# Performance work log

Measured on AMD Instinct MI355X. Metric: run time of the kernel, lower is better.

The kernel has to match this reference:

```python
import jax, jax.numpy as jnp
import numpy as np

X_DIM, H_DIM, Z_DIM = 4096, 4096, 512
EMB_DIM, NUM_EMB = 512, 8192
BATCH = 8192
COMMIT = 0.25


def setup_inputs() -> dict:
    key = jax.random.key(0)
    ks = jax.random.split(key, 12)
    s = 0.02
    return {
        "x": jax.random.normal(ks[0], (BATCH, X_DIM), dtype=jnp.float32),
        "enc_w1": jax.random.normal(ks[1], (X_DIM, H_DIM), dtype=jnp.float32) * s,
        "enc_b1": jnp.zeros((H_DIM,), dtype=jnp.float32),
        "enc_w2": jax.random.normal(ks[2], (H_DIM, Z_DIM), dtype=jnp.float32) * s,
        "enc_b2": jnp.zeros((Z_DIM,), dtype=jnp.float32),
        "pre_w": jax.random.normal(ks[3], (Z_DIM, EMB_DIM), dtype=jnp.float32) * s,
        "pre_b": jnp.zeros((EMB_DIM,), dtype=jnp.float32),
        "codebook": jax.random.normal(ks[4], (NUM_EMB, EMB_DIM), dtype=jnp.float32) * s,
        "dec_w1": jax.random.normal(ks[5], (EMB_DIM, H_DIM), dtype=jnp.float32) * s,
        "dec_b1": jnp.zeros((H_DIM,), dtype=jnp.float32),
        "dec_w2": jax.random.normal(ks[6], (H_DIM, X_DIM), dtype=jnp.float32) * s,
        "dec_b2": jnp.zeros((X_DIM,), dtype=jnp.float32),
    }


def reference(x, enc_w1, enc_b1, enc_w2, enc_b2, pre_w, pre_b, codebook,
              dec_w1, dec_b1, dec_w2, dec_b2):
    # Encoder MLP: Linear -> ReLU -> Linear
    h = jax.nn.relu(x @ enc_w1 + enc_b1)              # [B, H]
    z = h @ enc_w2 + enc_b2                           # [B, Z]
    z_e = z @ pre_w + pre_b                           # [B, E]

    # Vector quantization: nearest codebook entry by L2 distance
    # ||z||^2 - 2 z E^T + ||E||^2 over K codes
    d = (jnp.sum(z_e * z_e, axis=1, keepdims=True)
         - 2.0 * (z_e @ codebook.T)
         + jnp.sum(codebook * codebook, axis=1))      # [B, K]
    idx = jnp.argmin(d, axis=1)                       # [B]
    z_q = codebook[idx]                               # [B, E] gather

    # VQ losses
    e_latent = jnp.mean((jax.lax.stop_gradient(z_q) - z_e) ** 2)
    q_latent = jnp.mean((z_q - jax.lax.stop_gradient(z_e)) ** 2)
    vq_loss = q_latent + COMMIT * e_latent

    # Perplexity of code usage
    counts = jnp.zeros((NUM_EMB,), dtype=jnp.float32).at[idx].add(1.0)
    avg_probs = counts / z_e.shape[0]
    perplexity = jnp.exp(-jnp.sum(avg_probs * jnp.log(avg_probs + 1e-10)))

    # Straight-through estimator
    z_st = z_e + jax.lax.stop_gradient(z_q - z_e)

    # Decoder MLP
    hd = jax.nn.relu(z_st @ dec_w1 + dec_b1)
    x_recon = hd @ dec_w2 + dec_b2                    # [B, X]
    return (x_recon, vq_loss, perplexity)
```

## Files before the change

### kernel.cpp

```cpp
#include <hip/hip_runtime.h>
#include <cstdint>
#include <cstddef>


#define BM 128
#define BN 128
#define BKT 16
#define LDA 132
#define LDB 132

typedef _Float16 half_t;
typedef __attribute__((ext_vector_type(8))) _Float16 f16x8;
typedef __attribute__((ext_vector_type(4))) _Float16 f16x4;
typedef __attribute__((ext_vector_type(4))) float floatx4;
typedef __attribute__((ext_vector_type(8))) short bf16x8;

#define LO_SCALE 4096.f
#define LO_INV   2.44140625e-4f

__device__ __forceinline__ short f2bf(float v) {
    union { float f; unsigned u; } x; x.f = v;
    unsigned r = x.u + 0x7fff + ((x.u >> 16) & 1);
    return (short)(r >> 16);
}

__device__ __forceinline__ void gload16(const void* g, void* l) {
    __builtin_amdgcn_global_load_lds(
        (const __attribute__((address_space(1))) void*)(uintptr_t)g,
        (__attribute__((address_space(3))) void*)(uintptr_t)l,
        16, 0, 0);
}

__device__ __forceinline__ void fsplit(float v, half_t& hi, half_t& lo) {
    hi = (half_t)v;
    lo = (half_t)((v - (float)hi) * LO_SCALE);
}

__global__ __launch_bounds__(256, 2)
void gemm_bias_act(const float* __restrict__ A, const float* __restrict__ B,
                   const float* __restrict__ bias, float* __restrict__ C,
                   int M, int N, int K, int relu)
{
    __shared__ float as[BKT][LDA];
    __shared__ float bs[BKT][LDB];
    const int tid = threadIdx.x;
    const int tx = tid & 15;
    const int ty = tid >> 4;
    const int row0 = blockIdx.y * BM;
    const int col0 = blockIdx.x * BN;

    const int ar = tid >> 2;
    const int ac = (tid & 3) << 2;
    const int br = tid >> 5;
    const int bc = (tid & 31) << 2;

    const float* Ap0 = A + (size_t)(row0 + ar) * K + ac;
    const float* Ap1 = A + (size_t)(row0 + ar + 64) * K + ac;
    const float* Bp0 = B + (size_t)br * N + col0 + bc;
    const float* Bp1 = B + (size_t)(br + 8) * N + col0 + bc;

    float acc[8][8];
#pragma unroll
    for (int i = 0; i < 8; ++i)
#pragma unroll
        for (int j = 0; j < 8; ++j) acc[i][j] = 0.f;

    for (int k0 = 0; k0 < K; k0 += BKT) {
        float4 a0 = *(const float4*)(Ap0 + k0);
        float4 a1 = *(const float4*)(Ap1 + k0);
        float4 b0 = *(const float4*)(Bp0 + (size_t)k0 * N);
        float4 b1 = *(const float4*)(Bp1 + (size_t)k0 * N);
        __syncthreads();
        as[ac + 0][ar] = a0.x; as[ac + 1][ar] = a0.y;
        as[ac + 2][ar] = a0.z; as[ac + 3][ar] = a0.w;
        as[ac + 0][ar + 64] = a1.x; as[ac + 1][ar + 64] = a1.y;
        as[ac + 2][ar + 64] = a1.z; as[ac + 3][ar + 64] = a1.w;
        *(float4*)&bs[br][bc] = b0;
        *(float4*)&bs[br + 8][bc] = b1;
        __syncthreads();
#pragma unroll
        for (int k = 0; k < BKT; ++k) {
            float af[8], bf0[4], bf1[4];
            *(float4*)&af[0] = *(const float4*)&as[k][ty * 8];
            *(float4*)&af[4] = *(const float4*)&as[k][ty * 8 + 4];
            *(float4*)&bf0[0] = *(const float4*)&bs[k][tx * 4];
            *(float4*)&bf1[0] = *(const float4*)&bs[k][64 + tx * 4];
#pragma unroll
            for (int i = 0; i < 8; ++i) {
#pragma unroll
                for (int j = 0; j < 4; ++j) {
                    acc[i][j]     = fmaf(af[i], bf0[j], acc[i][j]);
                    acc[i][j + 4] = fmaf(af[i], bf1[j], acc[i][j + 4]);
                }
            }
        }
    }

    float bv0[4], bv1[4];
#pragma unroll
    for (int j = 0; j < 4; ++j) {
        bv0[j] = bias[col0 + tx * 4 + j];
        bv1[j] = bias[col0 + 64 + tx * 4 + j];
    }
#pragma unroll
    for (int i = 0; i < 8; ++i) {
        const int row = row0 + ty * 8 + i;
        float4 o0, o1;
        o0.x = acc[i][0] + bv0[0]; o0.y = acc[i][1] + bv0[1];
        o0.z = acc[i][2] + bv0[2]; o0.w = acc[i][3] + bv0[3];
        o1.x = acc[i][4] + bv1[0]; o1.y = acc[i][5] + bv1[1];
        o1.z = acc[i][6] + bv1[2]; o1.w = acc[i][7] + bv1[3];
        if (relu) {
            o0.x = fmaxf(o0.x, 0.f); o0.y = fmaxf(o0.y, 0.f);
            o0.z = fmaxf(o0.z, 0.f); o0.w = fmaxf(o0.w, 0.f);
            o1.x = fmaxf(o1.x, 0.f); o1.y = fmaxf(o1.y, 0.f);
            o1.z = fmaxf(o1.z, 0.f); o1.w = fmaxf(o1.w, 0.f);
        }
        *(float4*)(C + (size_t)row * N + col0 + tx * 4) = o0;
        *(float4*)(C + (size_t)row * N + col0 + 64 + tx * 4) = o1;
    }
}

__global__ void cnorm_kernel(const float* __restrict__ CB, float* __restrict__ cnorm, int E)
{
    const int j = blockIdx.x;
    const float* c = CB + (size_t)j * E;
    float s = 0.f;
    for (int e = threadIdx.x; e < E; e += 64) { float v = c[e]; s += v * v; }
#pragma unroll
    for (int off = 32; off; off >>= 1) s += __shfl_down(s, off);
    if (threadIdx.x == 0) cnorm[j] = s;
}

__global__ void argmin_reduce(const float* __restrict__ partv, const int* __restrict__ parti,
                              int* __restrict__ idx, int M, int P)
{
    const int m = blockIdx.x * blockDim.x + threadIdx.x;
    if (m >= M) return;
    const float* pv = partv + (size_t)m * P;
    const int* pi = parti + (size_t)m * P;
    float best = pv[0]; int bi = pi[0];
    for (int t = 1; t < P; ++t) {
        float v = pv[t]; int ii = pi[t];
        if (v < best || (v == best && ii < bi)) { best = v; bi = ii; }
    }
    idx[m] = bi;
}

__global__ __launch_bounds__(256)
void vq_stats(const float* __restrict__ ZE, const float* __restrict__ CB,
              const int* __restrict__ idx, int* __restrict__ counts,
              float* __restrict__ vqaccum, int E)
{
    const int i = blockIdx.x;
    const int id = idx[i];
    const float* c = CB + (size_t)id * E;
    const float* z = ZE + (size_t)i * E;
    float s = 0.f;
    for (int e = threadIdx.x; e < E; e += 256) { float d = c[e] - z[e]; s += d * d; }
#pragma unroll
    for (int off = 32; off; off >>= 1) s += __shfl_down(s, off);
    __shared__ float red[4];
    const int lane = threadIdx.x & 63, w = threadIdx.x >> 6;
    if (lane == 0) red[w] = s;
    __syncthreads();
    if (threadIdx.x == 0) {
        atomicAdd(vqaccum, red[0] + red[1] + red[2] + red[3]);
        atomicAdd(counts + id, 1);
    }
}

__global__ void zero_kernel(int* __restrict__ p, int n)
{
    const int i = blockIdx.x * 256 + threadIdx.x;
    if (i < n) p[i] = 0;
}

__global__ __launch_bounds__(256)
void finalize(const int* __restrict__ counts, const float* __restrict__ vqaccum,
              float* __restrict__ tail, int NCODE, float invB, float scale)
{
    float s = 0.f;
    for (int j = threadIdx.x; j < NCODE; j += 256) {
        float p = (float)counts[j] * invB;
        s += p * logf(p + 1e-10f);
    }
#pragma unroll
    for (int off = 32; off; off >>= 1) s += __shfl_down(s, off);
    __shared__ float red[4];
    const int lane = threadIdx.x & 63, w = threadIdx.x >> 6;
    if (lane == 0) red[w] = s;
    __syncthreads();
    if (threadIdx.x == 0) {
        tail[0] = vqaccum[0] * scale;
        tail[1] = expf(-(red[0] + red[1] + red[2] + red[3]));
    }
}

__global__ __launch_bounds__(256)
void transpose_bf16(const float* __restrict__ src, short* __restrict__ dst,
                    int Kd, int Nd)
{
    __shared__ float tile[32][33];
    const int bx = blockIdx.x * 32;
    const int by = blockIdx.y * 32;
    const int tx = threadIdx.x & 31, ty = threadIdx.x >> 5;
#pragma unroll
    for (int i = ty; i < 32; i += 8)
        tile[i][tx] = src[(size_t)(by + i) * Nd + bx + tx];
    __syncthreads();
#pragma unroll
    for (int i = ty; i < 32; i += 8)
        dst[(size_t)(bx + i) * Kd + by + tx] = f2bf(tile[tx][i]);
}

__global__ __launch_bounds__(256)
void transpose_split2(const float* __restrict__ src, half_t* __restrict__ dh,
                      half_t* __restrict__ dl, int Kd, int Nd)
{
    __shared__ float tile[32][33];
    const int bx = blockIdx.x * 32;
    const int by = blockIdx.y * 32;
    const int tx = threadIdx.x & 31, ty = threadIdx.x >> 5;
#pragma unroll
    for (int i = ty; i < 32; i += 8)
        tile[i][tx] = src[(size_t)(by + i) * Nd + bx + tx];
    __syncthreads();
#pragma unroll
    for (int i = ty; i < 32; i += 8) {
        float v = tile[tx][i];
        half_t h, l; fsplit(v, h, l);
        dh[(size_t)(bx + i) * Kd + by + tx] = h;
        dl[(size_t)(bx + i) * Kd + by + tx] = l;
    }
}

__global__ void convert_bf16_vec(const float* __restrict__ src, short* __restrict__ dst, int n4)
{
    const int i = blockIdx.x * 256 + threadIdx.x;
    if (i >= n4) return;
    float4 v = ((const float4*)src)[i];
    short4 o;
    o.x = f2bf(v.x); o.y = f2bf(v.y); o.z = f2bf(v.z); o.w = f2bf(v.w);
    ((short4*)dst)[i] = o;
}

__global__ void split2_vec(const float* __restrict__ src, half_t* __restrict__ hi,
                           half_t* __restrict__ lo, int n4)
{
    const int i = blockIdx.x * 256 + threadIdx.x;
    if (i >= n4) return;
    float4 v = ((const float4*)src)[i];
    f16x4 h, l;
    h[0] = (half_t)v.x; l[0] = (half_t)((v.x - (float)h[0]) * LO_SCALE);
    h[1] = (half_t)v.y; l[1] = (half_t)((v.y - (float)h[1]) * LO_SCALE);
    h[2] = (half_t)v.z; l[2] = (half_t)((v.z - (float)h[2]) * LO_SCALE);
    h[3] = (half_t)v.w; l[3] = (half_t)((v.w - (float)h[3]) * LO_SCALE);
    ((f16x4*)hi)[i] = h;
    ((f16x4*)lo)[i] = l;
}

template<int MODE>
__global__ __launch_bounds__(256, 2)
void gemm_f16x2(const half_t* __restrict__ Ah, const half_t* __restrict__ Al,
                const half_t* __restrict__ Bh, const half_t* __restrict__ Bl,
                const float* __restrict__ bias, float* __restrict__ Cf,
                half_t* __restrict__ Ch, half_t* __restrict__ Cl,
                int N, int K)
{
    __shared__ half_t sAh[128 * 32], sAl[128 * 32], sBh[128 * 32], sBl[128 * 32];
    const int t = threadIdx.x;
    const int lane = t & 63, wave = t >> 6;
    const int rh = (wave >> 1) * 64, ch = (wave & 1) * 64;
    const int ml = lane & 15, quad = lane >> 4;
    const int row0 = blockIdx.y * 128, col0 = blockIdx.x * 128;

    const int r = t >> 2, c = t & 3;
    const half_t* pA0h = Ah + (size_t)(row0 + r) * K + c * 8;
    const half_t* pA1h = Ah + (size_t)(row0 + r + 64) * K + c * 8;
    const half_t* pA0l = Al + (size_t)(row0 + r) * K + c * 8;
    const half_t* pA1l = Al + (size_t)(row0 + r + 64) * K + c * 8;
    const half_t* pB0h = Bh + (size_t)(col0 + r) * K + c * 8;
    const half_t* pB1h = Bh + (size_t)(col0 + r + 64) * K + c * 8;
    const half_t* pB0l = Bl + (size_t)(col0 + r) * K + c * 8;
    const half_t* pB1l = Bl + (size_t)(col0 + r + 64) * K + c * 8;
    half_t* dA0h = sAh + (r * 4 + c) * 8;  half_t* dA1h = sAh + ((r + 64) * 4 + c) * 8;
    half_t* dA0l = sAl + (r * 4 + c) * 8;  half_t* dA1l = sAl + ((r + 64) * 4 + c) * 8;
    half_t* dB0h = sBh + (r * 4 + c) * 8;  half_t* dB1h = sBh + ((r + 64) * 4 + c) * 8;
    half_t* dB0l = sBl + (r * 4 + c) * 8;  half_t* dB1l = sBl + ((r + 64) * 4 + c) * 8;

    floatx4 acc_h[4][4] = {};
    floatx4 acc_c[4][4] = {};

    for (int k0 = 0; k0 < K; k0 += 32) {
        __syncthreads();
        gload16(pA0h + k0, dA0h); gload16(pA1h + k0, dA1h);
        gload16(pA0l + k0, dA0l); gload16(pA1l + k0, dA1l);
        gload16(pB0h + k0, dB0h); gload16(pB1h + k0, dB1h);
        gload16(pB0l + k0, dB0l); gload16(pB1l + k0, dB1l);
        __syncthreads();
        f16x8 ah[4], alo[4], bh[4], blo[4];
#pragma unroll
        for (int i = 0; i < 4; ++i) {
            ah[i]  = *(const f16x8*)(sAh + (rh + i * 16 + ml) * 32 + quad * 8);
            alo[i] = *(const f16x8*)(sAl + (rh + i * 16 + ml) * 32 + quad * 8);
        }
#pragma unroll
        for (int j = 0; j < 4; ++j) {
            bh[j]  = *(const f16x8*)(sBh + (ch + j * 16 + ml) * 32 + quad * 8);
            blo[j] = *(const f16x8*)(sBl + (ch + j * 16 + ml) * 32 + quad * 8);
        }
#pragma unroll
        for (int i = 0; i < 4; ++i)
#pragma unroll
            for (int j = 0; j < 4; ++j) {
                acc_h[i][j] = __builtin_amdgcn_mfma_f32_16x16x32_f16(ah[i],  bh[j],  acc_h[i][j], 0, 0, 0);
                acc_c[i][j] = __builtin_amdgcn_mfma_f32_16x16x32_f16(ah[i],  blo[j], acc_c[i][j], 0, 0, 0);
                acc_c[i][j] = __builtin_amdgcn_mfma_f32_16x16x32_f16(alo[i], bh[j],  acc_c[i][j], 0, 0, 0);
            }
    }

    float bv[4];
#pragma unroll
    for (int j = 0; j < 4; ++j) bv[j] = bias[col0 + ch + j * 16 + ml];
#pragma unroll
    for (int i = 0; i < 4; ++i) {
#pragma unroll
        for (int j = 0; j < 4; ++j) {
            const int col = col0 + ch + j * 16 + ml;
#pragma unroll
            for (int reg = 0; reg < 4; ++reg) {
                const int row = row0 + rh + i * 16 + quad * 4 + reg;
                float v = fmaf(acc_c[i][j][reg], LO_INV, acc_h[i][j][reg]) + bv[j];
                if (MODE == 0) {
                    Cf[(size_t)row * N + col] = v;
                } else {
                    v = fmaxf(v, 0.f);
                    half_t hh = (half_t)v;
                    Ch[(size_t)row * N + col] = hh;
                    Cl[(size_t)row * N + col] = (half_t)((v - (float)hh) * LO_SCALE);
                }
            }
        }
    }
}

__global__ __launch_bounds__(256, 2)
void dist_f16x2_argmin(const half_t* __restrict__ Ah, const half_t* __restrict__ Al,
                       const half_t* __restrict__ Bh, const half_t* __restrict__ Bl,
                       const float* __restrict__ cnorm, float* __restrict__ partv,
                       int* __restrict__ parti, int K)
{
    __shared__ half_t smem[4 * 128 * 32];
    half_t* sAh = smem;
    half_t* sAl = smem + 4096;
    half_t* sBh = smem + 8192;
    half_t* sBl = smem + 12288;

    const int t = threadIdx.x;
    const int lane = t & 63, wave = t >> 6;
    const int rh = (wave >> 1) * 64, ch = (wave & 1) * 64;
    const int ml = lane & 15, quad = lane >> 4;
    const int row0 = blockIdx.y * 128, col0 = blockIdx.x * 128;

    const int r = t >> 2, c = t & 3;
    const half_t* pA0h = Ah + (size_t)(row0 + r) * K + c * 8;
    const half_t* pA1h = Ah + (size_t)(row0 + r + 64) * K + c * 8;
    const half_t* pA0l = Al + (size_t)(row0 + r) * K + c * 8;
    const half_t* pA1l = Al + (size_t)(row0 + r + 64) * K + c * 8;
    const half_t* pB0h = Bh + (size_t)(col0 + r) * K + c * 8;
    const half_t* pB1h = Bh + (size_t)(col0 + r + 64) * K + c * 8;
    const half_t* pB0l = Bl + (size_t)(col0 + r) * K + c * 8;
    const half_t* pB1l = Bl + (size_t)(col0 + r + 64) * K + c * 8;
    half_t* dA0h = sAh + (r * 4 + c) * 8;  half_t* dA1h = sAh + ((r + 64) * 4 + c) * 8;
    half_t* dA0l = sAl + (r * 4 + c) * 8;  half_t* dA1l = sAl + ((r + 64) * 4 + c) * 8;
    half_t* dB0h = sBh + (r * 4 + c) * 8;  half_t* dB1h = sBh + ((r + 64) * 4 + c) * 8;
    half_t* dB0l = sBl + (r * 4 + c) * 8;  half_t* dB1l = sBl + ((r + 64) * 4 + c) * 8;

    floatx4 acc_h[4][4] = {};
    floatx4 acc_c[4][4] = {};

    for (int k0 = 0; k0 < K; k0 += 32) {
        __syncthreads();
        gload16(pA0h + k0, dA0h); gload16(pA1h + k0, dA1h);
        gload16(pA0l + k0, dA0l); gload16(pA1l + k0, dA1l);
        gload16(pB0h + k0, dB0h); gload16(pB1h + k0, dB1h);
        gload16(pB0l + k0, dB0l); gload16(pB1l + k0, dB1l);
        __syncthreads();
        f16x8 ah[4], alo[4], bh[4], blo[4];
#pragma unroll
        for (int i = 0; i < 4; ++i) {
            ah[i]  = *(const f16x8*)(sAh + (rh + i * 16 + ml) * 32 + quad * 8);
            alo[i] = *(const f16x8*)(sAl + (rh + i * 16 + ml) * 32 + quad * 8);
        }
#pragma unroll
        for (int j = 0; j < 4; ++j) {
            bh[j]  = *(const f16x8*)(sBh + (ch + j * 16 + ml) * 32 + quad * 8);
            blo[j] = *(const f16x8*)(sBl + (ch + j * 16 + ml) * 32 + quad * 8);
        }
#pragma unroll
        for (int i = 0; i < 4; ++i)
#pragma unroll
            for (int j = 0; j < 4; ++j) {
                acc_h[i][j] = __builtin_amdgcn_mfma_f32_16x16x32_f16(ah[i],  bh[j],  acc_h[i][j], 0, 0, 0);
                acc_c[i][j] = __builtin_amdgcn_mfma_f32_16x16x32_f16(ah[i],  blo[j], acc_c[i][j], 0, 0, 0);
                acc_c[i][j] = __builtin_amdgcn_mfma_f32_16x16x32_f16(alo[i], bh[j],  acc_c[i][j], 0, 0, 0);
            }
    }

    float cnv[4];
#pragma unroll
    for (int j = 0; j < 4; ++j) cnv[j] = cnorm[col0 + ch + j * 16 + ml];

    __syncthreads();
    float* rv = (float*)smem;
    int*   ri = (int*)(smem + 8192);
    const int slot = (wave & 1) * 16 + ml;

#pragma unroll
    for (int i = 0; i < 4; ++i) {
#pragma unroll
        for (int reg = 0; reg < 4; ++reg) {
            const int lr = rh + i * 16 + quad * 4 + reg;
            float best = __builtin_inff(); int bi = 0;
#pragma unroll
            for (int j = 0; j < 4; ++j) {
                float s = fmaf(acc_c[i][j][reg], LO_INV, acc_h[i][j][reg]);
                float v = cnv[j] - 2.f * s;
                if (v < best) { best = v; bi = col0 + ch + j * 16 + ml; }
            }
            rv[lr * 32 + slot] = best;
            ri[lr * 32 + slot] = bi;
        }
    }
    __syncthreads();
    if (t < 128) {
        float best = __builtin_inff(); int bi = 0x7fffffff;
        for (int s = 0; s < 32; ++s) {
            const int sl = (s + t) & 31;
            float v = rv[t * 32 + sl]; int ii = ri[t * 32 + sl];
            if (v < best || (v == best && ii < bi)) { best = v; bi = ii; }
        }
        partv[(size_t)(row0 + t) * gridDim.x + blockIdx.x] = best;
        parti[(size_t)(row0 + t) * gridDim.x + blockIdx.x] = bi;
    }
}

template<int RELU, int OUT_BF16, int GATHER>
__global__ __launch_bounds__(256)
void mfma_gemm_bt(const short* __restrict__ A, const short* __restrict__ BT,
                  const float* __restrict__ bias, float* __restrict__ Cf,
                  short* __restrict__ Cb, int M, int N, int K,
                  const int* __restrict__ rowidx)
{
    __shared__ short sA[128 * 32];
    __shared__ short sB[128 * 32];
    const int t = threadIdx.x;
    const int lane = t & 63;
    const int wave = t >> 6;
    const int rh = (wave >> 1) * 64;
    const int ch = (wave & 1) * 64;
    const int ml = lane & 15;
    const int quad = lane >> 4;
    const int row0 = blockIdx.y * 128, col0 = blockIdx.x * 128;

    const int r = t >> 2;
    const int c = t & 3;
    int ga0 = row0 + r, ga1 = row0 + r + 64;
    if (GATHER) { ga0 = rowidx[ga0]; ga1 = rowidx[ga1]; }
    const short* pA0 = A + (size_t)ga0 * K + c * 8;
    const short* pA1 = A + (size_t)ga1 * K + c * 8;
    const short* pB0 = BT + (size_t)(col0 + r) * K + c * 8;
    const short* pB1 = BT + (size_t)(col0 + r + 64) * K + c * 8;
    short* dA0 = sA + (r * 4 + c) * 8;
    short* dA1 = sA + ((r + 64) * 4 + c) * 8;
    short* dB0 = sB + (r * 4 + c) * 8;
    short* dB1 = sB + ((r + 64) * 4 + c) * 8;

    floatx4 acc[4][4] = {};

    for (int k0 = 0; k0 < K; k0 += 32) {
        __syncthreads();
        gload16(pA0 + k0, dA0);
        gload16(pA1 + k0, dA1);
        gload16(pB0 + k0, dB0);
        gload16(pB1 + k0, dB1);
        __syncthreads();
        bf16x8 af[4], bf[4];
#pragma unroll
        for (int i = 0; i < 4; ++i)
            af[i] = *(const bf16x8*)(sA + ((rh + i * 16 + ml) * 32 + quad * 8));
#pragma unroll
        for (int j = 0; j < 4; ++j)
            bf[j] = *(const bf16x8*)(sB + ((ch + j * 16 + ml) * 32 + quad * 8));
#pragma unroll
        for (int i = 0; i < 4; ++i)
#pragma unroll
            for (int j = 0; j < 4; ++j)
                acc[i][j] = __builtin_amdgcn_mfma_f32_16x16x32_bf16(
                    af[i], bf[j], acc[i][j], 0, 0, 0);
    }

    float bv[4];
#pragma unroll
    for (int j = 0; j < 4; ++j) bv[j] = bias[col0 + ch + j * 16 + ml];
#pragma unroll
    for (int i = 0; i < 4; ++i) {
#pragma unroll
        for (int j = 0; j < 4; ++j) {
            const int col = col0 + ch + j * 16 + ml;
#pragma unroll
            for (int reg = 0; reg < 4; ++reg) {
                const int row = row0 + rh + i * 16 + quad * 4 + reg;
                float v = acc[i][j][reg] + bv[j];
                if (RELU) v = fmaxf(v, 0.f);
                if (OUT_BF16) Cb[(size_t)row * N + col] = f2bf(v);
                else          Cf[(size_t)row * N + col] = v;
            }
        }
    }
}

extern "C" void kernel_launch(void* const* d_in, const int* in_sizes, int n_in,
                              void* d_out, int out_size, void* d_ws, size_t ws_size,
                              hipStream_t stream)
{
    const float* x      = (const float*)d_in[0];
    const float* enc_w1 = (const float*)d_in[1];
    const float* enc_b1 = (const float*)d_in[2];
    const float* enc_w2 = (const float*)d_in[3];
    const float* enc_b2 = (const float*)d_in[4];
    const float* pre_w  = (const float*)d_in[5];
    const float* pre_b  = (const float*)d_in[6];
    const float* cb     = (const float*)d_in[7];
    const float* dec_w1 = (const float*)d_in[8];
    const float* dec_b1 = (const float*)d_in[9];
    const float* dec_w2 = (const float*)d_in[10];
    const float* dec_b2 = (const float*)d_in[11];
    float* out = (float*)d_out;

    const int B = 8192, X = 4096, H = 4096, Z = 512, E = 512, NC = 8192;

    char* w = (char*)d_ws;
    half_t* xh   = (half_t*)(w);
    half_t* xl   = (half_t*)(w + 67108864ull);
    half_t* w1Th = (half_t*)(w + 134217728ull);
    half_t* w1Tl = (half_t*)(w + 167772160ull);
    half_t* w2Th = (half_t*)(w + 201326592ull);
    half_t* w2Tl = (half_t*)(w + 205520896ull);

    half_t* hhp  = (half_t*)d_out;
    half_t* hlp  = (half_t*)((char*)d_out + 67108864ull);

    float*  z    = (float*)(w);
    float*  ze   = (float*)(w + 16777216ull);
    half_t* zeh  = (half_t*)(w + 33554432ull);
    half_t* zel  = (half_t*)(w + 41943040ull);
    half_t* cbh  = (half_t*)(w + 50331648ull);
    half_t* cbl  = (half_t*)(w + 58720256ull);
    short*  hd_bf= (short*)(w + 67108864ull);

    short*  dw1T = (short*)(w + 134217728ull);
    short*  dw2T = (short*)(w + 138412032ull);
    short*  cb_bf= (short*)(w + 171966464ull);

    float*  cn   = (float*)(w + 201326592ull);
    float*  pv   = (float*)(w + 201359360ull);
    int*    pi   = (int*)  (w + 203456512ull);
    int*    idx  = (int*)  (w + 205553664ull);
    int*    cnt  = (int*)  (w + 205586432ull);
    float*  vqa  = (float*)(w + 205619200ull);

    dim3 blk(256);

    split2_vec<<<(B * X / 4 + 255) / 256, blk, 0, stream>>>(x, xh, xl, B * X / 4);
    transpose_split2<<<dim3(H / 32, X / 32), blk, 0, stream>>>(enc_w1, w1Th, w1Tl, X, H);
    transpose_split2<<<dim3(Z / 32, H / 32), blk, 0, stream>>>(enc_w2, w2Th, w2Tl, H, Z);

    gemm_f16x2<1><<<dim3(H / 128, B / 128), blk, 0, stream>>>(
        xh, xl, w1Th, w1Tl, enc_b1, nullptr, hhp, hlp, H, X);
    gemm_f16x2<0><<<dim3(Z / 128, B / 128), blk, 0, stream>>>(
        hhp, hlp, w2Th, w2Tl, enc_b2, z, nullptr, nullptr, Z, H);
    gemm_bias_act<<<dim3(E / BN, B / BM), blk, 0, stream>>>(z, pre_w, pre_b, ze, B, E, Z, 0);

    split2_vec<<<(B * E / 4 + 255) / 256, blk, 0, stream>>>(ze, zeh, zel, B * E / 4);
    split2_vec<<<(NC * E / 4 + 255) / 256, blk, 0, stream>>>(cb, cbh, cbl, NC * E / 4);
    cnorm_kernel<<<NC, 64, 0, stream>>>(cb, cn, E);
    zero_kernel<<<(NC + 1 + 255) / 256, blk, 0, stream>>>(cnt, NC + 1);
    dist_f16x2_argmin<<<dim3(NC / 128, B / 128), blk, 0, stream>>>(
        zeh, zel, cbh, cbl, cn, pv, pi, E);
    argmin_reduce<<<B / 256, blk, 0, stream>>>(pv, pi, idx, B, NC / 128);
    vq_stats<<<B, blk, 0, stream>>>(ze, cb, idx, cnt, vqa, E);

    convert_bf16_vec<<<(NC * E / 4 + 255) / 256, blk, 0, stream>>>(cb, cb_bf, NC * E / 4);
    transpose_bf16<<<dim3(H / 32, E / 32), blk, 0, stream>>>(dec_w1, dw1T, E, H);
    transpose_bf16<<<dim3(X / 32, H / 32), blk, 0, stream>>>(dec_w2, dw2T, H, X);
    mfma_gemm_bt<1, 1, 1><<<dim3(H / 128, B / 128), blk, 0, stream>>>(
        cb_bf, dw1T, dec_b1, nullptr, hd_bf, B, H, E, idx);
    mfma_gemm_bt<0, 0, 0><<<dim3(X / 128, B / 128), blk, 0, stream>>>(
        hd_bf, dw2T, dec_b2, out, nullptr, B, X, H, nullptr);

    finalize<<<1, blk, 0, stream>>>(cnt, vqa, out + (out_size - 2), NC,
                                    1.f / (float)B, 1.25f / ((float)B * (float)E));
}
```

Measured before the change: 2.286 ms.

## Replace encoder first GEMM with 512-thread triple-buffered phased MFMA kernel

```diff
diff --git a/kernel.cpp b/kernel.cpp
--- a/kernel.cpp
+++ b/kernel.cpp
@@ -35,6 +35,19 @@
     hi = (half_t)v;
     lo = (half_t)((v - (float)hi) * LO_SCALE);
 }
+
+#define MFMA16F(a, b, c) __builtin_amdgcn_mfma_f32_16x16x32_f16((a), (b), (c), 0, 0, 0)
+
+#define SBARRIER() do { \
+    __builtin_amdgcn_sched_barrier(0); \
+    __builtin_amdgcn_s_barrier(); \
+    __builtin_amdgcn_sched_barrier(0); \
+} while (0)
+
+#define LGKM0() do { \
+    asm volatile("s_waitcnt lgkmcnt(0)" ::: "memory"); \
+    __builtin_amdgcn_sched_barrier(0); \
+} while (0)
 
 __global__ __launch_bounds__(256, 2)
 void gemm_bias_act(const float* __restrict__ A, const float* __restrict__ B,
@@ -260,6 +273,161 @@
     ((f16x4*)lo)[i] = l;
 }
 
+#define E1_BUF 49152
+#define E1_AH  0
+#define E1_AL  16384
+#define E1_BH  32768
+#define E1_BL  40960
+
+__global__ __launch_bounds__(512, 2)
+void enc1_8ph(const half_t* __restrict__ Ah, const half_t* __restrict__ Al,
+              const half_t* __restrict__ Bh, const half_t* __restrict__ Bl,
+              const float* __restrict__ bias,
+              half_t* __restrict__ Ch, half_t* __restrict__ Cl,
+              int N, int K)
+{
+    __shared__ char smem[3 * E1_BUF];
+    const int t = threadIdx.x;
+    const int lane = t & 63, wave = t >> 6;
+    const int wm = wave >> 1;
+    const int wn = wave & 1;
+    const int ml = lane & 15, quad = lane >> 4;
+    const int row0 = blockIdx.y * 256, col0 = blockIdx.x * 128;
+
+    const int rowA = t & 255;
+    const int kqA0 = t >> 8;
+    const int rowB = t & 127;
+    const int kqB  = t >> 7;
+    const half_t* gAh0 = Ah + (size_t)(row0 + rowA) * K + kqA0 * 8;
+    const half_t* gAh1 = gAh0 + 16;
+    const half_t* gAl0 = Al + (size_t)(row0 + rowA) * K + kqA0 * 8;
+    const half_t* gAl1 = gAl0 + 16;
+    const half_t* gBhp = Bh + (size_t)(col0 + rowB) * K + kqB * 8;
+    const half_t* gBlp = Bl + (size_t)(col0 + rowB) * K + kqB * 8;
+    const int dA0 = t * 16;
+    const int dA1 = (512 + t) * 16;
+    const int dB  = t * 16;
+
+    const int aoff = ((quad << 8) + wm * 64 + ml) * 16;
+    const int boff = ((quad << 7) + wn * 64 + ml) * 16;
+
+    floatx4 acc_h[4][4] = {};
+    floatx4 acc_c[4][4] = {};
+
+    const int NT = K >> 5;
+    int ro = 0, mo = E1_BUF, wo = 2 * E1_BUF;
+
+    {
+        char* b0 = smem;
+        char* b1 = smem + E1_BUF;
+        gload16(gAh0, b0 + E1_AH + dA0);  gload16(gAh1, b0 + E1_AH + dA1);
+        gload16(gAl0, b0 + E1_AL + dA0);  gload16(gAl1, b0 + E1_AL + dA1);
+        gload16(gBhp, b0 + E1_BH + dB );  gload16(gBlp, b0 + E1_BL + dB );
+        gload16(gAh0 + 32, b1 + E1_AH + dA0);  gload16(gAh1 + 32, b1 + E1_AH + dA1);
+        gload16(gAl0 + 32, b1 + E1_AL + dA0);  gload16(gAl1 + 32, b1 + E1_AL + dA1);
+        gload16(gBhp + 32, b1 + E1_BH + dB );  gload16(gBlp + 32, b1 + E1_BL + dB );
+    }
+    asm volatile("s_waitcnt vmcnt(6)" ::: "memory");
+    SBARRIER();
+
+    for (int kt = 0; kt < NT; ++kt) {
+        const int stage = (kt + 2 < NT);
+        const size_t ks = (size_t)(kt + 2) * 32;
+        char* rb = smem + ro;
+        char* wb = smem + wo;
+        f16x8 bhf[4], blf[4], ahf, alf;
+
+#pragma unroll
+        for (int j = 0; j < 4; ++j) {
+            bhf[j] = *(const f16x8*)(rb + E1_BH + boff + j * 256);
+            blf[j] = *(const f16x8*)(rb + E1_BL + boff + j * 256);
+        }
+        ahf = *(const f16x8*)(rb + E1_AH + aoff + 0 * 256);
+        alf = *(const f16x8*)(rb + E1_AL + aoff + 0 * 256);
+        if (stage) { gload16(gAh0 + ks, wb + E1_AH + dA0);
+                     gload16(gAh1 + ks, wb + E1_AH + dA1); }
+        SBARRIER(); LGKM0();
+        __builtin_amdgcn_s_setprio(1);
+#pragma unroll
+        for (int j = 0; j < 4; ++j) acc_h[0][j] = MFMA16F(ahf, bhf[j], acc_h[0][j]);
+#pragma unroll
+        for (int j = 0; j < 4; ++j) acc_c[0][j] = MFMA16F(ahf, blf[j], acc_c[0][j]);
+#pragma unroll
+        for (int j = 0; j < 4; ++j) acc_c[0][j] = MFMA16F(alf, bhf[j], acc_c[0][j]);
+        __builtin_amdgcn_s_setprio(0);
+        SBARRIER();
+
+        ahf = *(const f16x8*)(rb + E1_AH + aoff + 1 * 256);
+        alf = *(const f16x8*)(rb + E1_AL + aoff + 1 * 256);
+        if (stage) { gload16(gAl0 + ks, wb + E1_AL + dA0);
+                     gload16(gAl1 + ks, wb + E1_AL + dA1); }
+        SBARRIER(); LGKM0();
+        __builtin_amdgcn_s_setprio(1);
+#pragma unroll
+        for (int j = 0; j < 4; ++j) acc_h[1][j] = MFMA16F(ahf, bhf[j], acc_h[1][j]);
+#pragma unroll
+        for (int j = 0; j < 4; ++j) acc_c[1][j] = MFMA16F(ahf, blf[j], acc_c[1][j]);
+#pragma unroll
+        for (int j = 0; j < 4; ++j) acc_c[1][j] = MFMA16F(alf, bhf[j], acc_c[1][j]);
+        __builtin_amdgcn_s_setprio(0);
+        SBARRIER();
+
+        ahf = *(const f16x8*)(rb + E1_AH + aoff + 2 * 256);
+        alf = *(const f16x8*)(rb + E1_AL + aoff + 2 * 256);
+        if (stage) { gload16(gBhp + ks, wb + E1_BH + dB);
+                     gload16(gBlp + ks, wb + E1_BL + dB); }
+        SBARRIER(); LGKM0();
+        __builtin_amdgcn_s_setprio(1);
+#pragma unroll
+        for (int j = 0; j < 4; ++j) acc_h[2][j] = MFMA16F(ahf, bhf[j], acc_h[2][j]);
+#pragma unroll
+        for (int j = 0; j < 4; ++j) acc_c[2][j] = MFMA16F(ahf, blf[j], acc_c[2][j]);
+#pragma unroll
+        for (int j = 0; j < 4; ++j) acc_c[2][j] = MFMA16F(alf, bhf[j], acc_c[2][j]);
+        __builtin_amdgcn_s_setprio(0);
+        SBARRIER();
+
+        ahf = *(const f16x8*)(rb + E1_AH + aoff + 3 * 256);
+        alf = *(const f16x8*)(rb + E1_AL + aoff + 3 * 256);
+        SBARRIER(); LGKM0();
+        __builtin_amdgcn_s_setprio(1);
+#pragma unroll
+        for (int j = 0; j < 4; ++j) acc_h[3][j] = MFMA16F(ahf, bhf[j], acc_h[3][j]);
+#pragma unroll
+        for (int j = 0; j < 4; ++j) acc_c[3][j] = MFMA16F(ahf, blf[j], acc_c[3][j]);
+#pragma unroll
+        for (int j = 0; j < 4; ++j) acc_c[3][j] = MFMA16F(alf, bhf[j], acc_c[3][j]);
+        __builtin_amdgcn_s_setprio(0);
+
+        if (kt + 1 < NT) {
+            if (stage) { asm volatile("s_waitcnt vmcnt(6)" ::: "memory"); }
+            else       { asm volatile("s_waitcnt vmcnt(0)" ::: "memory"); }
+            SBARRIER();
+        }
+        const int tmp = ro; ro = mo; mo = wo; wo = tmp;
+    }
+
+    float bv[4];
+#pragma unroll
+    for (int j = 0; j < 4; ++j) bv[j] = bias[col0 + wn * 64 + j * 16 + ml];
+#pragma unroll
+    for (int i = 0; i < 4; ++i) {
+#pragma unroll
+        for (int j = 0; j < 4; ++j) {
+            const int col = col0 + wn * 64 + j * 16 + ml;
+#pragma unroll
+            for (int reg = 0; reg < 4; ++reg) {
+                const int row = row0 + wm * 64 + i * 16 + quad * 4 + reg;
+                float v = fmaf(acc_c[i][j][reg], LO_INV, acc_h[i][j][reg]) + bv[j];
+                v = fmaxf(v, 0.f);
+                half_t hh = (half_t)v;
+                Ch[(size_t)row * N + col] = hh;
+                Cl[(size_t)row * N + col] = (half_t)((v - (float)hh) * LO_SCALE);
+            }
+        }
+    }
+}
+
 template<int MODE>
 __global__ __launch_bounds__(256, 2)
 void gemm_f16x2(const half_t* __restrict__ Ah, const half_t* __restrict__ Al,
@@ -314,9 +482,9 @@
         for (int i = 0; i < 4; ++i)
 #pragma unroll
             for (int j = 0; j < 4; ++j) {
-                acc_h[i][j] = __builtin_amdgcn_mfma_f32_16x16x32_f16(ah[i],  bh[j],  acc_h[i][j], 0, 0, 0);
-                acc_c[i][j] = __builtin_amdgcn_mfma_f32_16x16x32_f16(ah[i],  blo[j], acc_c[i][j], 0, 0, 0);
-                acc_c[i][j] = __builtin_amdgcn_mfma_f32_16x16x32_f16(alo[i], bh[j],  acc_c[i][j], 0, 0, 0);
+                acc_h[i][j] = MFMA16F(ah[i],  bh[j],  acc_h[i][j]);
+                acc_c[i][j] = MFMA16F(ah[i],  blo[j], acc_c[i][j]);
+                acc_c[i][j] = MFMA16F(alo[i], bh[j],  acc_c[i][j]);
             }
     }
 
@@ -324,7 +492,7 @@
 #pragma unroll
     for (int j = 0; j < 4; ++j) bv[j] = bias[col0 + ch + j * 16 + ml];
 #pragma unroll
-    for (int i = 0; i < 4; ++i) {
+    for (int i = 0; i < 4; ++i)
 #pragma unroll
         for (int j = 0; j < 4; ++j) {
             const int col = col0 + ch + j * 16 + ml;
@@ -342,7 +510,6 @@
                 }
             }
         }
-    }
 }
 
 __global__ __launch_bounds__(256, 2)
@@ -402,9 +569,9 @@
         for (int i = 0; i < 4; ++i)
 #pragma unroll
             for (int j = 0; j < 4; ++j) {
-                acc_h[i][j] = __builtin_amdgcn_mfma_f32_16x16x32_f16(ah[i],  bh[j],  acc_h[i][j], 0, 0, 0);
-                acc_c[i][j] = __builtin_amdgcn_mfma_f32_16x16x32_f16(ah[i],  blo[j], acc_c[i][j], 0, 0, 0);
-                acc_c[i][j] = __builtin_amdgcn_mfma_f32_16x16x32_f16(alo[i], bh[j],  acc_c[i][j], 0, 0, 0);
+                acc_h[i][j] = MFMA16F(ah[i],  bh[j],  acc_h[i][j]);
+                acc_c[i][j] = MFMA16F(ah[i],  blo[j], acc_c[i][j]);
+                acc_c[i][j] = MFMA16F(alo[i], bh[j],  acc_c[i][j]);
             }
     }
 
@@ -577,8 +744,8 @@
     transpose_split2<<<dim3(H / 32, X / 32), blk, 0, stream>>>(enc_w1, w1Th, w1Tl, X, H);
     transpose_split2<<<dim3(Z / 32, H / 32), blk, 0, stream>>>(enc_w2, w2Th, w2Tl, H, Z);
 
-    gemm_f16x2<1><<<dim3(H / 128, B / 128), blk, 0, stream>>>(
-        xh, xl, w1Th, w1Tl, enc_b1, nullptr, hhp, hlp, H, X);
+    enc1_8ph<<<dim3(H / 128, B / 256), dim3(512), 0, stream>>>(
+        xh, xl, w1Th, w1Tl, enc_b1, hhp, hlp, H, X);
     gemm_f16x2<0><<<dim3(Z / 128, B / 128), blk, 0, stream>>>(
         hhp, hlp, w2Th, w2Tl, enc_b2, z, nullptr, nullptr, Z, H);
     gemm_bias_act<<<dim3(E / BN, B / BM), blk, 0, stream>>>(z, pre_w, pre_b, ze, B, E, Z, 0);
```

Result: slower. 2.526 ms (+10.5%).
